# Performance work log

Hardware: AMD Instinct MI355X
Metric: run time of the kernel (lower is better)

## Reference

```python
import jax, jax.numpy as jnp
import numpy as np

N_NODES = 100000
N_GRAPHS = 256
EPS = 1e-5


def setup_inputs() -> dict:
    key = jax.random.key(0)
    ks = jax.random.split(key, 16)
    x = jax.random.normal(ks[0], (N_NODES, 7), dtype=jnp.float32)
    edge_index = jax.random.randint(ks[1], (2, 1600000), 0, N_NODES, dtype=jnp.int64)
    batch = jnp.sort(jax.random.randint(ks[2], (N_NODES,), 0, N_GRAPHS, dtype=jnp.int64))

    def lin(k, fi, fo):
        s = 1.0 / np.sqrt(fi)
        kw, kb = jax.random.split(k)
        W = jax.random.uniform(kw, (fi, fo), jnp.float32, -s, s)
        b = jax.random.uniform(kb, (fo,), jnp.float32, -s, s)
        return W, b

    W1, b1 = lin(ks[3], 7, 71)
    W2, b2 = lin(ks[4], 71, 135)
    W3, b3 = lin(ks[5], 135, 199)
    Wl1, bl1 = lin(ks[6], 199, 49)
    Wl2, bl2 = lin(ks[7], 49, 2)
    return {
        "x": x, "edge_index": edge_index, "batch": batch,
        "bn0_g": jnp.ones((7,)), "bn0_b": jnp.zeros((7,)),
        "bn1_g": jnp.ones((71,)), "bn1_b": jnp.zeros((71,)),
        "bn2_g": jnp.ones((135,)), "bn2_b": jnp.zeros((135,)),
        "W1": W1, "b1": b1, "W2": W2, "b2": b2, "W3": W3, "b3": b3,
        "Wl1": Wl1, "bl1": bl1, "Wl2": Wl2, "bl2": bl2,
    }


def _bn(x, g, b):
    # BatchNorm1d in training mode: batch stats over node dim
    m = jnp.mean(x, axis=0)
    v = jnp.mean(jnp.square(x - m), axis=0)
    return (x - m) * jax.lax.rsqrt(v + EPS) * g + b


def _gcn(x, src, dst, norm, W, b):
    # PyG GCNConv: x' = D^{-1/2} (A+I) D^{-1/2} (x W) + b
    h = x @ W
    out = jax.ops.segment_sum(norm[:, None] * h[src], dst, num_segments=N_NODES)
    return out + b


def reference(x, edge_index, batch, bn0_g, bn0_b, bn1_g, bn1_b, bn2_g, bn2_b,
              W1, b1, W2, b2, W3, b3, Wl1, bl1, Wl2, bl2):
    # add self loops
    loops = jnp.arange(N_NODES, dtype=edge_index.dtype)
    src = jnp.concatenate([edge_index[0], loops])
    dst = jnp.concatenate([edge_index[1], loops])
    deg = jax.ops.segment_sum(jnp.ones_like(dst, dtype=x.dtype), dst, num_segments=N_NODES)
    d_isqrt = jax.lax.rsqrt(jnp.maximum(deg, 1.0))
    norm = d_isqrt[src] * d_isqrt[dst]

    h = _bn(x, bn0_g, bn0_b)
    h = jax.nn.relu(_gcn(h, src, dst, norm, W1, b1))
    h = _bn(h, bn1_g, bn1_b)
    h = jax.nn.relu(_gcn(h, src, dst, norm, W2, b2))
    h = _bn(h, bn2_g, bn2_b)
    h = jax.nn.relu(_gcn(h, src, dst, norm, W3, b3))

    # global mean pool over graphs
    sums = jax.ops.segment_sum(h, batch, num_segments=N_GRAPHS)
    cnts = jax.ops.segment_sum(jnp.ones((h.shape[0],), h.dtype), batch, num_segments=N_GRAPHS)
    pooled = sums / jnp.maximum(cnts, 1.0)[:, None]

    out = pooled @ Wl1 + bl1
    out = out @ Wl2 + bl2
    return out
```

## Files before the change

kernel.cpp:

```cpp
#include <hip/hip_runtime.h>
#include <hip/hip_fp16.h>

#define EPSV 1e-5f
#define BIN_CH 4096
#define BCAP 8192

typedef _Float16 f16;
typedef f16 half8 __attribute__((ext_vector_type(8)));
typedef float f32x4 __attribute__((ext_vector_type(4)));


__global__ __launch_bounds__(256) void k_bin(const int* __restrict__ src,
                                             const int* __restrict__ dst, int E, int EN,
                                             int NBK, int* __restrict__ gcur,
                                             int* __restrict__ binned) {
    __shared__ int cnt[512];
    __shared__ int base[512];
    for (int b = threadIdx.x; b < 512; b += 256) cnt[b] = 0;
    __syncthreads();
    int i0 = blockIdx.x * BIN_CH;
    int i1 = i0 + BIN_CH; if (i1 > EN) i1 = EN;
    for (int i = i0 + threadIdx.x; i < i1; i += 256) {
        int d = (i < E) ? dst[i] : (i - E);
        atomicAdd(&cnt[d >> 8], 1);
    }
    __syncthreads();
    for (int b = threadIdx.x; b < NBK; b += 256)
        if (cnt[b]) base[b] = b * BCAP + atomicAdd(&gcur[b], cnt[b]);
    __syncthreads();
    for (int i = i0 + threadIdx.x; i < i1; i += 256) {
        int s, d;
        if (i < E) { s = src[i]; d = dst[i]; }
        else       { s = i - E; d = s; }
        int pos = atomicAdd(&base[d >> 8], 1);
        binned[pos] = s | ((d & 255) << 24);
    }
}

__global__ __launch_bounds__(256) void k_bucket(const int* __restrict__ binned,
                                                const int* __restrict__ gcur, int N,
                                                int* __restrict__ deg, int* __restrict__ rs,
                                                int* __restrict__ csr_s,
                                                float* __restrict__ disq) {
    __shared__ int deg_l[256];
    __shared__ int sc[256];
    __shared__ int cur_l[256];
    int b = blockIdx.x;
    int t = threadIdx.x;
    int start = b * BCAP, end = start + gcur[b];
    deg_l[t] = 0;
    __syncthreads();
    for (int i = start + t; i < end; i += 256)
        atomicAdd(&deg_l[((unsigned)binned[i]) >> 24], 1);
    __syncthreads();
    sc[t] = deg_l[t];
    __syncthreads();
    for (int off = 1; off < 256; off <<= 1) {
        int v = (t >= off) ? sc[t - off] : 0;
        __syncthreads();
        sc[t] += v;
        __syncthreads();
    }
    int rs_l = sc[t] - deg_l[t];
    int n = b * 256 + t;
    if (n < N) {
        deg[n] = deg_l[t];
        rs[n] = start + rs_l;
        disq[n] = rsqrtf((float)(deg_l[t] > 0 ? deg_l[t] : 1));
    }
    cur_l[t] = start + rs_l;
    __syncthreads();
    for (int i = start + t; i < end; i += 256) {
        int p = binned[i];
        int loc = ((unsigned)p) >> 24;
        int idx = atomicAdd(&cur_l[loc], 1);
        csr_s[idx] = p & 0xFFFFFF;
    }
}

__global__ __launch_bounds__(256) void k_wfill(const int* __restrict__ rs,
                                               const int* __restrict__ deg,
                                               const int* __restrict__ csr_s,
                                               const float* __restrict__ disq,
                                               int2* __restrict__ csr_sw, int N) {
    int wave = threadIdx.x >> 6, lane = threadIdx.x & 63;
    int n = blockIdx.x * 4 + wave;
    if (n >= N) return;
    int e0 = rs[n], dg = deg[n];
    float dn = disq[n];
    for (int j = lane; j < dg; j += 64) {
        int s = csr_s[e0 + j];
        int2 sw;
        sw.x = s;
        sw.y = __float_as_int(disq[s] * dn);
        csr_sw[e0 + j] = sw;
    }
}


__global__ __launch_bounds__(256) void k_prep(
    const float* __restrict__ colsum, const float* __restrict__ colsq,
    const float* __restrict__ g, const float* __restrict__ b, float invN,
    const float* __restrict__ W, int Cin, int Cout, int KP,
    f16* __restrict__ Wp, float* __restrict__ wrow) {
    __shared__ float lsc[192];
    __shared__ float lsh[192];
    __shared__ float red[4];
    int t = threadIdx.x;
    int c = blockIdx.x;
    if (t < KP) {
        float scv = 0.f, shv = 0.f;
        if (t < Cin) {
            float m = colsum[t] * invN;
            float v = colsq[t] * invN - m * m;
            float rstd = rsqrtf(fmaxf(v, 0.f) + EPSV);
            scv = rstd * g[t];
            shv = b[t] - m * scv;
        }
        lsc[t] = scv; lsh[t] = shv;
    }
    __syncthreads();
    float part = 0.f;
    if (t < KP) {
        float wv = (t < Cin && c < Cout) ? W[(size_t)t * Cout + c] : 0.f;
        Wp[(size_t)c * KP + t] = (f16)(lsc[t] * wv);
        part = lsh[t] * wv;
    }
    for (int off = 32; off > 0; off >>= 1) part += __shfl_down(part, off);
    int lane = t & 63, wid = t >> 6;
    if (lane == 0) red[wid] = part;
    __syncthreads();
    if (t == 0) wrow[c] = red[0] + red[1] + red[2] + red[3];
}


__global__ __launch_bounds__(256) void k_padx_stats(const float* __restrict__ x,
                                                    __half* __restrict__ xp, int N,
                                                    float* __restrict__ colsum,
                                                    float* __restrict__ colsq,
                                                    const int* __restrict__ batch,
                                                    int* __restrict__ gstart,
                                                    int* __restrict__ gend) {
    __shared__ float ls[16];
    int t = threadIdx.x;
    int n = blockIdx.x * 256 + t;
    int lane = t & 63;
    if (t < 16) ls[t] = 0.f;
    __syncthreads();
    float v[7] = {0.f, 0.f, 0.f, 0.f, 0.f, 0.f, 0.f};
    if (n < N) {
#pragma unroll
        for (int j = 0; j < 7; ++j) v[j] = x[(size_t)n * 7 + j];
        __half h[8];
#pragma unroll
        for (int j = 0; j < 7; ++j) h[j] = __float2half(v[j]);
        h[7] = __float2half(0.f);
        *(float4*)(xp + (size_t)n * 8) = *(float4*)h;
        int g = batch[n];
        int gp = (n == 0) ? -1 : batch[n - 1];
        if (gp != g) gstart[g] = n;
        int gn = (n == N - 1) ? -1 : batch[n + 1];
        if (gn != g) gend[g] = n + 1;
    }
#pragma unroll
    for (int j = 0; j < 7; ++j) {
        float s = v[j];
        float q = v[j] * v[j];
        for (int off = 32; off > 0; off >>= 1) {
            s += __shfl_down(s, off);
            q += __shfl_down(q, off);
        }
        if (lane == 0) {
            atomicAdd(&ls[j], s);
            atomicAdd(&ls[8 + j], q);
        }
    }
    __syncthreads();
    if (t < 8)               atomicAdd(&colsum[t], ls[t]);
    else if (t < 16)         atomicAdd(&colsq[t - 8], ls[t]);
}


__global__ void k_gather8(const __half* __restrict__ xp, const int2* __restrict__ csr_sw,
                          const int* __restrict__ rs, const int* __restrict__ deg,
                          __half* __restrict__ out, float* __restrict__ rsum, int N) {
    int n = blockIdx.x * blockDim.x + threadIdx.x;
    if (n >= N) return;
    int e0 = rs[n], eend = e0 + deg[n];
    float a0 = 0.f, a1 = 0.f, a2 = 0.f, a3 = 0.f, a4 = 0.f, a5 = 0.f, a6 = 0.f, a7 = 0.f;
    float ws = 0.f;
    for (int e = e0; e < eend; ++e) {
        int2 sw = csr_sw[e];
        float w = __int_as_float(sw.y);
        ws += w;
        float4 r = *(const float4*)(xp + (size_t)sw.x * 8);
        const __half2* hh = (const __half2*)&r;
        float2 q0 = __half22float2(hh[0]);
        float2 q1 = __half22float2(hh[1]);
        float2 q2 = __half22float2(hh[2]);
        float2 q3 = __half22float2(hh[3]);
        a0 = fmaf(w, q0.x, a0); a1 = fmaf(w, q0.y, a1);
        a2 = fmaf(w, q1.x, a2); a3 = fmaf(w, q1.y, a3);
        a4 = fmaf(w, q2.x, a4); a5 = fmaf(w, q2.y, a5);
        a6 = fmaf(w, q3.x, a6); a7 = fmaf(w, q3.y, a7);
    }
    rsum[n] = ws;
    __half h[8];
    h[0] = __float2half(a0); h[1] = __float2half(a1);
    h[2] = __float2half(a2); h[3] = __float2half(a3);
    h[4] = __float2half(a4); h[5] = __float2half(a5);
    h[6] = __float2half(a6); h[7] = __float2half(a7);
    *(float4*)(out + (size_t)n * 8) = *(float4*)h;
}


__global__ __launch_bounds__(256) void k_gemm_mfma(
    const f16* __restrict__ A, int SPa,
    const f16* __restrict__ Bt, int KP,
    const float* __restrict__ rsum, const float* __restrict__ wrow,
    const float* __restrict__ bias,
    f16* __restrict__ outM, int SPm, int MAIN, f16* __restrict__ outT, int TOTW,
    float* __restrict__ colsum, float* __restrict__ colsq, int do_stats,
    int N, int Cout) {
    __shared__ f16 As[128][40];
    __shared__ float s_sum[64];
    __shared__ float s_sq[64];
    const int r0 = blockIdx.x * 128;
    const int c0 = blockIdx.y * 64;
    const int t = threadIdx.x;
    const int wave = t >> 6, lane = t & 63;
    const int l15 = lane & 15, quad = lane >> 4;

    if (t < 64) { s_sum[t] = 0.f; s_sq[t] = 0.f; }

    f32x4 zero4 = {0.f, 0.f, 0.f, 0.f};
    f32x4 acc[2][4];
#pragma unroll
    for (int mi = 0; mi < 2; ++mi)
#pragma unroll
        for (int ni = 0; ni < 4; ++ni) acc[mi][ni] = zero4;

    const int KT = KP >> 5;
    for (int kt = 0; kt < KT; ++kt) {
        int k0 = kt * 32;
        {
            int kcol = (t & 7) * 4;
            int rbase = t >> 3;
            int gk = k0 + kcol;
            bool kok = (gk + 4 <= SPa);
#pragma unroll
            for (int i = 0; i < 4; ++i) {
                int row = rbase + i * 32;
                int gr = r0 + row;
                ushort4 v = {0, 0, 0, 0};
                if (gr < N && kok)
                    v = *(const ushort4*)(A + (size_t)gr * SPa + gk);
                *(ushort4*)&As[row][kcol] = v;
            }
        }
        __syncthreads();
        half8 a0 = *(const half8*)&As[wave * 32 + l15][quad * 8];
        half8 a1 = *(const half8*)&As[wave * 32 + 16 + l15][quad * 8];
#pragma unroll
        for (int ni = 0; ni < 4; ++ni) {
            half8 b = *(const half8*)(Bt + (size_t)(c0 + ni * 16 + l15) * KP + k0 + quad * 8);
            acc[0][ni] = __builtin_amdgcn_mfma_f32_16x16x32_f16(a0, b, acc[0][ni], 0, 0, 0);
            acc[1][ni] = __builtin_amdgcn_mfma_f32_16x16x32_f16(a1, b, acc[1][ni], 0, 0, 0);
        }
        __syncthreads();
    }

    float wr[4], bi[4];
#pragma unroll
    for (int ni = 0; ni < 4; ++ni) {
        int gc = c0 + ni * 16 + l15;
        wr[ni] = wrow[gc];
        bi[ni] = (gc < Cout) ? bias[gc] : 0.f;
    }
    float ps[4] = {}, pq[4] = {};
#pragma unroll
    for (int mi = 0; mi < 2; ++mi) {
#pragma unroll
        for (int reg = 0; reg < 4; ++reg) {
            int gr = r0 + wave * 32 + mi * 16 + quad * 4 + reg;
            if (gr >= N) continue;
            float rsv = rsum[gr];
#pragma unroll
            for (int ni = 0; ni < 4; ++ni) {
                int gc = c0 + ni * 16 + l15;
                float o = acc[mi][ni][reg] + rsv * wr[ni] + bi[ni];
                o = fmaxf(o, 0.f);
                if (gc >= Cout) o = 0.f;
                ps[ni] += o; pq[ni] += o * o;
                if (gc < MAIN) {
                    if (gc < TOTW) outM[(size_t)gr * SPm + gc] = (f16)o;
                } else if (gc < TOTW) {
                    outT[(size_t)gr * 8 + (gc - MAIN)] = (f16)o;
                }
            }
        }
    }
    if (do_stats) {
#pragma unroll
        for (int ni = 0; ni < 4; ++ni) {
            int cl = ni * 16 + l15;
            atomicAdd(&s_sum[cl], ps[ni]);
            atomicAdd(&s_sq[cl], pq[ni]);
        }
        __syncthreads();
        if (t < 64 && c0 + t < Cout) {
            atomicAdd(&colsum[c0 + t], s_sum[t]);
            atomicAdd(&colsq[c0 + t], s_sq[t]);
        }
    }
}

__device__ __forceinline__ void fma8(float* acc, float w, float4 r) {
    float2 q0 = __half22float2(((const __half2*)&r)[0]);
    float2 q1 = __half22float2(((const __half2*)&r)[1]);
    float2 q2 = __half22float2(((const __half2*)&r)[2]);
    float2 q3 = __half22float2(((const __half2*)&r)[3]);
    acc[0] = fmaf(w, q0.x, acc[0]); acc[1] = fmaf(w, q0.y, acc[1]);
    acc[2] = fmaf(w, q1.x, acc[2]); acc[3] = fmaf(w, q1.y, acc[3]);
    acc[4] = fmaf(w, q2.x, acc[4]); acc[5] = fmaf(w, q2.y, acc[5]);
    acc[6] = fmaf(w, q3.x, acc[6]); acc[7] = fmaf(w, q3.y, acc[7]);
}

__device__ __forceinline__ void gather_walk(const __half* __restrict__ gb, int SPM,
                                            const int2* __restrict__ csr_sw,
                                            int e0, int eend, float* acc) {
    if (e0 >= eend) return;
    int2 cur[8];
#pragma unroll
    for (int i = 0; i < 8; ++i) cur[i] = csr_sw[e0 + i];
    for (int e = e0; e < eend; ) {
        int en = e + 8;
        int2 nxt[8];
#pragma unroll
        for (int i = 0; i < 8; ++i) nxt[i] = csr_sw[en + i];
        float4 r[8];
#pragma unroll
        for (int i = 0; i < 8; ++i) {
            int si = (e + i < eend) ? cur[i].x : 0;
            r[i] = *(const float4*)(gb + (size_t)si * SPM);
        }
#pragma unroll
        for (int i = 0; i < 8; ++i) {
            float w = (e + i < eend) ? __int_as_float(cur[i].y) : 0.f;
            fma8(acc, w, r[i]);
        }
#pragma unroll
        for (int i = 0; i < 8; ++i) cur[i] = nxt[i];
        e = en;
    }
}


__global__ __launch_bounds__(256) void k_fused2(
    const __half* __restrict__ Am, const __half* __restrict__ At,
    const f16* __restrict__ Bt,
    const int* __restrict__ rs, const int* __restrict__ deg,
    const int2* __restrict__ csr_sw,
    const float* __restrict__ rsum, const float* __restrict__ wrow,
    const float* __restrict__ bias,
    f16* __restrict__ outM, f16* __restrict__ outT,
    float* __restrict__ colsum, float* __restrict__ colsq, int N) {
    const int KP = 96, ASW = 104, SPM = 64, COUT = 135;
    __shared__ f16 As[64][104];
    __shared__ float rsum_l[64];
    const int r0 = blockIdx.x * 64;
    const int t = threadIdx.x;
    const int wave = t >> 6, lane = t & 63;
    const int l15 = lane & 15, quad = lane >> 4;

    if (t < 64) rsum_l[t] = (r0 + t < N) ? rsum[r0 + t] : 0.f;
    {
        float4 z = {0.f, 0.f, 0.f, 0.f};
        for (int i = t; i < 64 * ASW / 8; i += 256) ((float4*)As)[i] = z;
    }
    __syncthreads();

    {
        const int sub = lane >> 3, lsub = lane & 7;
        const __half* gb = Am + lsub * 8;
        for (int pass = 0; pass < 2; ++pass) {
            int lrow = wave * 16 + pass * 8 + sub;
            int n = r0 + lrow;
            float acc[8] = {};
            if (n < N) gather_walk(gb, SPM, csr_sw, rs[n], rs[n] + deg[n], acc);
            __half2 h[4];
            h[0] = __floats2half2_rn(acc[0], acc[1]);
            h[1] = __floats2half2_rn(acc[2], acc[3]);
            h[2] = __floats2half2_rn(acc[4], acc[5]);
            h[3] = __floats2half2_rn(acc[6], acc[7]);
            *(float4*)&As[lrow][lsub * 8] = *(float4*)h;
        }
    }
    {
        const int p = lane >> 2, sl = lane & 3;
        int lrow = wave * 16 + p;
        int n = r0 + lrow;
        float acc[8] = {};
        if (n < N) {
            int eend = rs[n] + deg[n];
            for (int e = rs[n] + sl; e < eend; e += 4) {
                int2 sw = csr_sw[e];
                fma8(acc, __int_as_float(sw.y), *(const float4*)(At + (size_t)sw.x * 8));
            }
        }
#pragma unroll
        for (int j = 0; j < 8; ++j) {
            acc[j] += __shfl_xor(acc[j], 1);
            acc[j] += __shfl_xor(acc[j], 2);
        }
        if (sl == 0) {
            __half2 h[4];
            h[0] = __floats2half2_rn(acc[0], acc[1]);
            h[1] = __floats2half2_rn(acc[2], acc[3]);
            h[2] = __floats2half2_rn(acc[4], acc[5]);
            h[3] = __floats2half2_rn(acc[6], acc[7]);
            *(float4*)&As[lrow][64] = *(float4*)h;
        }
    }
    __syncthreads();

    for (int ch = 0; ch < 3; ++ch) {
        const int gc = wave * 48 + ch * 16 + l15;
        f32x4 zero4 = {0.f, 0.f, 0.f, 0.f};
        f32x4 acc2[4];
#pragma unroll
        for (int mg = 0; mg < 4; ++mg) acc2[mg] = zero4;
#pragma unroll
        for (int kt = 0; kt < 3; ++kt) {
            int k0 = kt * 32;
            half8 b = *(const half8*)(Bt + (size_t)gc * KP + k0 + quad * 8);
#pragma unroll
            for (int mg = 0; mg < 4; ++mg) {
                half8 a = *(const half8*)&As[mg * 16 + l15][k0 + quad * 8];
                acc2[mg] = __builtin_amdgcn_mfma_f32_16x16x32_f16(a, b, acc2[mg], 0, 0, 0);
            }
        }
        float wr1 = wrow[gc];
        float bi1 = (gc < COUT) ? bias[gc] : 0.f;
        float ps = 0.f, pq = 0.f;
#pragma unroll
        for (int mg = 0; mg < 4; ++mg) {
#pragma unroll
            for (int reg = 0; reg < 4; ++reg) {
                int lrow = mg * 16 + quad * 4 + reg;
                int gr = r0 + lrow;
                float o = acc2[mg][reg] + rsum_l[lrow] * wr1 + bi1;
                o = fmaxf(o, 0.f);
                if (gc >= COUT || gr >= N) o = 0.f;
                ps += o; pq += o * o;
                if (gr < N) {
                    if (gc < 128)      outM[(size_t)gr * 128 + gc] = (f16)o;
                    else if (gc < 136) outT[(size_t)gr * 8 + (gc - 128)] = (f16)o;
                }
            }
        }
        ps += __shfl_down(ps, 32); ps += __shfl_down(ps, 16);
        pq += __shfl_down(pq, 32); pq += __shfl_down(pq, 16);
        if (lane < 16 && gc < COUT) {
            atomicAdd(&colsum[gc], ps);
            atomicAdd(&colsq[gc], pq);
        }
    }
}


__global__ __launch_bounds__(256) void k_fused3(
    const __half* __restrict__ Am, const __half* __restrict__ At,
    const f16* __restrict__ Bt,
    const int* __restrict__ rs, const int* __restrict__ deg,
    const int2* __restrict__ csr_sw,
    const float* __restrict__ rsum, const float* __restrict__ wrow,
    const float* __restrict__ bias, const int* __restrict__ batch,
    float* __restrict__ pooled, int N) {
    const int KP = 160, ASW = 168, SPM = 128, COUT = 199;
    __shared__ f16 As[64][168];
    __shared__ int sbat[64];
    __shared__ float rsum_l[64];
    const int r0 = blockIdx.x * 64;
    const int t = threadIdx.x;
    const int wave = t >> 6, lane = t & 63;
    const int l15 = lane & 15, quad = lane >> 4;

    if (t < 64) {
        int gr = r0 + t;
        sbat[t] = batch[(gr < N) ? gr : (N - 1)];
        rsum_l[t] = (gr < N) ? rsum[gr] : 0.f;
    }
    {
        float4 z = {0.f, 0.f, 0.f, 0.f};
        for (int i = t; i < 64 * ASW / 8; i += 256) ((float4*)As)[i] = z;
    }
    __syncthreads();

    {
        const int sub = lane >> 4, lsub = lane & 15;
        const __half* gb = Am + lsub * 8;
        for (int pass = 0; pass < 4; ++pass) {
            int lrow = wave * 16 + pass * 4 + sub;
            int n = r0 + lrow;
            float acc[8] = {};
            if (n < N) gather_walk(gb, SPM, csr_sw, rs[n], rs[n] + deg[n], acc);
            __half2 h[4];
            h[0] = __floats2half2_rn(acc[0], acc[1]);
            h[1] = __floats2half2_rn(acc[2], acc[3]);
            h[2] = __floats2half2_rn(acc[4], acc[5]);
            h[3] = __floats2half2_rn(acc[6], acc[7]);
            *(float4*)&As[lrow][lsub * 8] = *(float4*)h;
        }
    }
    {
        const int p = lane >> 2, sl = lane & 3;
        int lrow = wave * 16 + p;
        int n = r0 + lrow;
        float acc[8] = {};
        if (n < N) {
            int eend = rs[n] + deg[n];
            for (int e = rs[n] + sl; e < eend; e += 4) {
                int2 sw = csr_sw[e];
                fma8(acc, __int_as_float(sw.y), *(const float4*)(At + (size_t)sw.x * 8));
            }
        }
#pragma unroll
        for (int j = 0; j < 8; ++j) {
            acc[j] += __shfl_xor(acc[j], 1);
            acc[j] += __shfl_xor(acc[j], 2);
        }
        if (sl == 0) {
            __half2 h[4];
            h[0] = __floats2half2_rn(acc[0], acc[1]);
            h[1] = __floats2half2_rn(acc[2], acc[3]);
            h[2] = __floats2half2_rn(acc[4], acc[5]);
            h[3] = __floats2half2_rn(acc[6], acc[7]);
            *(float4*)&As[lrow][128] = *(float4*)h;
        }
    }
    __syncthreads();

    const int g0 = sbat[0];
    const int ng = sbat[63] - g0;
    unsigned gpack = 0;
#pragma unroll
    for (int i = 0; i < 16; ++i) {
        int lrow = (i >> 2) * 16 + quad * 4 + (i & 3);
        gpack |= (unsigned)(sbat[lrow] - g0) << (2 * i);
    }

    for (int ch = 0; ch < 2; ++ch) {
        const int cb = wave * 64 + ch * 32;
        f32x4 zero4 = {0.f, 0.f, 0.f, 0.f};
        f32x4 acc2[4][2];
#pragma unroll
        for (int mg = 0; mg < 4; ++mg) {
            acc2[mg][0] = zero4; acc2[mg][1] = zero4;
        }
#pragma unroll
        for (int kt = 0; kt < 5; ++kt) {
            int k0 = kt * 32;
            half8 b0 = *(const half8*)(Bt + (size_t)(cb + l15) * KP + k0 + quad * 8);
            half8 b1 = *(const half8*)(Bt + (size_t)(cb + 16 + l15) * KP + k0 + quad * 8);
#pragma unroll
            for (int mg = 0; mg < 4; ++mg) {
                half8 a = *(const half8*)&As[mg * 16 + l15][k0 + quad * 8];
                acc2[mg][0] = __builtin_amdgcn_mfma_f32_16x16x32_f16(a, b0, acc2[mg][0], 0, 0, 0);
                acc2[mg][1] = __builtin_amdgcn_mfma_f32_16x16x32_f16(a, b1, acc2[mg][1], 0, 0, 0);
            }
        }
        float wr[2], bi[2];
        int gcn[2];
#pragma unroll
        for (int ni = 0; ni < 2; ++ni) {
            gcn[ni] = cb + ni * 16 + l15;
            wr[ni] = wrow[gcn[ni]];
            bi[ni] = (gcn[ni] < COUT) ? bias[gcn[ni]] : 0.f;
        }
#pragma unroll
        for (int mg = 0; mg < 4; ++mg) {
#pragma unroll
            for (int reg = 0; reg < 4; ++reg) {
                int lrow = mg * 16 + quad * 4 + reg;
                bool rok = (r0 + lrow < N);
                float rsv = rsum_l[lrow];
#pragma unroll
                for (int ni = 0; ni < 2; ++ni) {
                    float o = acc2[mg][ni][reg] + rsv * wr[ni] + bi[ni];
                    o = fmaxf(o, 0.f);
                    acc2[mg][ni][reg] = (rok && gcn[ni] < COUT) ? o : 0.f;
                }
            }
        }
        for (int gg = 0; gg <= ng; ++gg) {
            float p0 = 0.f, p1 = 0.f;
#pragma unroll
            for (int i = 0; i < 16; ++i) {
                bool m = (((gpack >> (2 * i)) & 3u) == (unsigned)gg);
                int mg = i >> 2, reg = i & 3;
                p0 += m ? acc2[mg][0][reg] : 0.f;
                p1 += m ? acc2[mg][1][reg] : 0.f;
            }
            p0 += __shfl_down(p0, 32); p0 += __shfl_down(p0, 16);
            p1 += __shfl_down(p1, 32); p1 += __shfl_down(p1, 16);
            if (lane < 16) {
                int g = g0 + gg;
                if (gcn[0] < COUT && p0 != 0.f)
                    atomicAdd(&pooled[(size_t)g * COUT + gcn[0]], p0);
                if (gcn[1] < COUT && p1 != 0.f)
                    atomicAdd(&pooled[(size_t)g * COUT + gcn[1]], p1);
            }
        }
    }
}


__global__ void k_mlp(const float* __restrict__ pooled, const int* __restrict__ gstart,
                      const int* __restrict__ gend,
                      const float* __restrict__ Wl1, const float* __restrict__ bl1,
                      const float* __restrict__ Wl2, const float* __restrict__ bl2,
                      float* __restrict__ out, int C) {
    __shared__ float p[199];
    __shared__ float t1[49];
    int g = blockIdx.x;
    int cnt = gend[g] - gstart[g];
    float inv = 1.f / (float)(cnt > 1 ? cnt : 1);
    for (int k = threadIdx.x; k < C; k += blockDim.x) p[k] = pooled[g * C + k] * inv;
    __syncthreads();
    if (threadIdx.x < 49) {
        float acc = bl1[threadIdx.x];
        for (int k = 0; k < C; ++k) acc += p[k] * Wl1[k * 49 + threadIdx.x];
        t1[threadIdx.x] = acc;
    }
    __syncthreads();
    if (threadIdx.x < 2) {
        float acc = bl2[threadIdx.x];
        for (int k = 0; k < 49; ++k) acc += t1[k] * Wl2[k * 2 + threadIdx.x];
        out[g * 2 + threadIdx.x] = acc;
    }
}


extern "C" void kernel_launch(void* const* d_in, const int* in_sizes, int n_in,
                              void* d_out, int out_size, void* d_ws, size_t ws_size,
                              hipStream_t stream) {
    const float* x     = (const float*)d_in[0];
    const int*   ei    = (const int*)d_in[1];
    const int*   batch = (const int*)d_in[2];
    const float* bn0g = (const float*)d_in[3];
    const float* bn0b = (const float*)d_in[4];
    const float* bn1g = (const float*)d_in[5];
    const float* bn1b = (const float*)d_in[6];
    const float* bn2g = (const float*)d_in[7];
    const float* bn2b = (const float*)d_in[8];
    const float* W1  = (const float*)d_in[9];
    const float* b1  = (const float*)d_in[10];
    const float* W2  = (const float*)d_in[11];
    const float* b2  = (const float*)d_in[12];
    const float* W3  = (const float*)d_in[13];
    const float* b3  = (const float*)d_in[14];
    const float* Wl1 = (const float*)d_in[15];
    const float* bl1 = (const float*)d_in[16];
    const float* Wl2 = (const float*)d_in[17];
    const float* bl2 = (const float*)d_in[18];

    const int N = in_sizes[0] / 7;
    const int E = in_sizes[1] / 2;
    const int EN = E + N;
    const int G = out_size / 2;
    const int NB = (N + 255) / 256;
    const int NBK = (N + 255) / 256;
    const int NBIN = (EN + BIN_CH - 1) / BIN_CH;

    const int* src = ei;
    const int* dst = ei + E;

    char* w = (char*)d_ws;
    auto alloc = [&](size_t bytes) -> void* {
        void* p = (void*)w;
        w += ((bytes + 255) / 256) * 256;
        return p;
    };
    size_t szH1m = (size_t)N * 64 * sizeof(__half);
    size_t szH1t = (size_t)N * 8 * sizeof(__half);
    size_t szH2m = (size_t)N * 128 * sizeof(__half);
    size_t szH2t = (size_t)N * 8 * sizeof(__half);
    char* regA = (char*)alloc(szH1m + szH1t + szH2m + szH2t);
    __half* H1m = (__half*)regA;
    __half* H1t = (__half*)(regA + szH1m);
    __half* H2m = (__half*)(regA + szH1m + szH1t);
    __half* H2t = (__half*)(regA + szH1m + szH1t + szH2m);

    __half* bufG = (__half*)alloc((size_t)N * 8 * sizeof(__half));
    f16*    wp   = (f16*)  alloc((size_t)256 * 160 * sizeof(f16));
    float*  wrow = (float*)alloc(256 * sizeof(float));
    __half* xp   = (__half*)alloc((size_t)N * 8 * sizeof(__half));
    float* disq  = (float*)alloc((size_t)N * sizeof(float));
    float* rsum  = (float*)alloc((size_t)N * sizeof(float));
    int*   deg   = (int*)  alloc((size_t)N * sizeof(int));
    int*   rs    = (int*)  alloc((size_t)N * sizeof(int));
    int*   binned= (int*)  alloc((size_t)NBK * BCAP * sizeof(int));
    int*   csr_s = (int*)  alloc((size_t)NBK * BCAP * sizeof(int));
    int2*  csr_sw= (int2*) alloc((size_t)NBK * BCAP * sizeof(int2) + 256);
    float* colsum0 = (float*)alloc(256 * sizeof(float));
    float* colsq0  = (float*)alloc(256 * sizeof(float));
    float* colsumA = (float*)alloc(256 * sizeof(float));
    float* colsqA  = (float*)alloc(256 * sizeof(float));
    float* colsumB = (float*)alloc(256 * sizeof(float));
    float* colsqB  = (float*)alloc(256 * sizeof(float));
    int*   gcur    = (int*)  alloc(512 * sizeof(int));
    float* pooled  = (float*)alloc((size_t)G * 199 * sizeof(float));
    int*   gstart  = (int*)  alloc((size_t)G * sizeof(int));
    int*   gend    = (int*)  alloc((size_t)G * sizeof(int));

    size_t zbytes = 6 * 1024 + 2048 + (((size_t)G * 199 * sizeof(float) + 255) / 256) * 256;
    hipMemsetAsync(colsum0, 0, zbytes, stream);

    k_bin<<<NBIN, 256, 0, stream>>>(src, dst, E, EN, NBK, gcur, binned);
    k_bucket<<<NBK, 256, 0, stream>>>(binned, gcur, N, deg, rs, csr_s, disq);
    k_wfill<<<(N + 3) / 4, 256, 0, stream>>>(rs, deg, csr_s, disq, csr_sw, N);

    const int GB = (N + 127) / 128;
    const int GB64 = (N + 63) / 64;

    k_padx_stats<<<NB, 256, 0, stream>>>(x, xp, N, colsum0, colsq0, batch, gstart, gend);
    k_prep<<<128, 256, 0, stream>>>(colsum0, colsq0, bn0g, bn0b, 1.f / (float)N,
                                    W1, 7, 71, 32, wp, wrow);
    k_gather8<<<(N + 255) / 256, 256, 0, stream>>>(xp, csr_sw, rs, deg, bufG, rsum, N);
    {
        dim3 grid(GB, 2);
        k_gemm_mfma<<<grid, 256, 0, stream>>>((const f16*)bufG, 8, wp, 32, rsum, wrow, b1,
                                              (f16*)H1m, 64, 64, (f16*)H1t, 72,
                                              colsumA, colsqA, 1, N, 71);
    }
    k_prep<<<192, 256, 0, stream>>>(colsumA, colsqA, bn1g, bn1b, 1.f / (float)N,
                                    W2, 71, 135, 96, wp, wrow);
    k_fused2<<<GB64, 256, 0, stream>>>(H1m, H1t, wp, rs, deg, csr_sw,
                                       rsum, wrow, b2, (f16*)H2m, (f16*)H2t,
                                       colsumB, colsqB, N);
    k_prep<<<256, 256, 0, stream>>>(colsumB, colsqB, bn2g, bn2b, 1.f / (float)N,
                                    W3, 135, 199, 160, wp, wrow);
    k_fused3<<<GB64, 256, 0, stream>>>(H2m, H2t, wp, rs, deg, csr_sw,
                                       rsum, wrow, b3, batch, pooled, N);

    k_mlp<<<G, 64, 0, stream>>>(pooled, gstart, gend, Wl1, bl1, Wl2, bl2, (float*)d_out, 199);
}
```

Before: 442.9 us.

## Fuse layer-1 gather with MFMA GEMM and shrink fused tiles to 32 rows

Replaces the separate layer-1 gather kernel and MFMA GEMM kernel with one fused kernel. It gathers the 8-wide inputs into shared memory using 8 lanes per node, then runs the 71-column MFMA epilogue directly, so the intermediate buffer is never written to or read back from global memory. The fused2/fused3 kernels move from 64-row to 32-row tiles with launch_bounds(256,8), 8-lane tail gathers and a 6-deep edge prefetch instead of 8. This aims for more blocks and higher occupancy, at the cost of re-reading the weights in more blocks and issuing more atomics.

```diff
diff --git a/kernel.cpp b/kernel.cpp
--- a/kernel.cpp
+++ b/kernel.cpp
@@ -180,141 +180,6 @@
     else if (t < 16)         atomicAdd(&colsq[t - 8], ls[t]);
 }
 
-
-__global__ void k_gather8(const __half* __restrict__ xp, const int2* __restrict__ csr_sw,
-                          const int* __restrict__ rs, const int* __restrict__ deg,
-                          __half* __restrict__ out, float* __restrict__ rsum, int N) {
-    int n = blockIdx.x * blockDim.x + threadIdx.x;
-    if (n >= N) return;
-    int e0 = rs[n], eend = e0 + deg[n];
-    float a0 = 0.f, a1 = 0.f, a2 = 0.f, a3 = 0.f, a4 = 0.f, a5 = 0.f, a6 = 0.f, a7 = 0.f;
-    float ws = 0.f;
-    for (int e = e0; e < eend; ++e) {
-        int2 sw = csr_sw[e];
-        float w = __int_as_float(sw.y);
-        ws += w;
-        float4 r = *(const float4*)(xp + (size_t)sw.x * 8);
-        const __half2* hh = (const __half2*)&r;
-        float2 q0 = __half22float2(hh[0]);
-        float2 q1 = __half22float2(hh[1]);
-        float2 q2 = __half22float2(hh[2]);
-        float2 q3 = __half22float2(hh[3]);
-        a0 = fmaf(w, q0.x, a0); a1 = fmaf(w, q0.y, a1);
-        a2 = fmaf(w, q1.x, a2); a3 = fmaf(w, q1.y, a3);
-        a4 = fmaf(w, q2.x, a4); a5 = fmaf(w, q2.y, a5);
-        a6 = fmaf(w, q3.x, a6); a7 = fmaf(w, q3.y, a7);
-    }
-    rsum[n] = ws;
-    __half h[8];
-    h[0] = __float2half(a0); h[1] = __float2half(a1);
-    h[2] = __float2half(a2); h[3] = __float2half(a3);
-    h[4] = __float2half(a4); h[5] = __float2half(a5);
-    h[6] = __float2half(a6); h[7] = __float2half(a7);
-    *(float4*)(out + (size_t)n * 8) = *(float4*)h;
-}
-
-
-__global__ __launch_bounds__(256) void k_gemm_mfma(
-    const f16* __restrict__ A, int SPa,
-    const f16* __restrict__ Bt, int KP,
-    const float* __restrict__ rsum, const float* __restrict__ wrow,
-    const float* __restrict__ bias,
-    f16* __restrict__ outM, int SPm, int MAIN, f16* __restrict__ outT, int TOTW,
-    float* __restrict__ colsum, float* __restrict__ colsq, int do_stats,
-    int N, int Cout) {
-    __shared__ f16 As[128][40];
-    __shared__ float s_sum[64];
-    __shared__ float s_sq[64];
-    const int r0 = blockIdx.x * 128;
-    const int c0 = blockIdx.y * 64;
-    const int t = threadIdx.x;
-    const int wave = t >> 6, lane = t & 63;
-    const int l15 = lane & 15, quad = lane >> 4;
-
-    if (t < 64) { s_sum[t] = 0.f; s_sq[t] = 0.f; }
-
-    f32x4 zero4 = {0.f, 0.f, 0.f, 0.f};
-    f32x4 acc[2][4];
-#pragma unroll
-    for (int mi = 0; mi < 2; ++mi)
-#pragma unroll
-        for (int ni = 0; ni < 4; ++ni) acc[mi][ni] = zero4;
-
-    const int KT = KP >> 5;
-    for (int kt = 0; kt < KT; ++kt) {
-        int k0 = kt * 32;
-        {
-            int kcol = (t & 7) * 4;
-            int rbase = t >> 3;
-            int gk = k0 + kcol;
-            bool kok = (gk + 4 <= SPa);
-#pragma unroll
-            for (int i = 0; i < 4; ++i) {
-                int row = rbase + i * 32;
-                int gr = r0 + row;
-                ushort4 v = {0, 0, 0, 0};
-                if (gr < N && kok)
-                    v = *(const ushort4*)(A + (size_t)gr * SPa + gk);
-                *(ushort4*)&As[row][kcol] = v;
-            }
-        }
-        __syncthreads();
-        half8 a0 = *(const half8*)&As[wave * 32 + l15][quad * 8];
-        half8 a1 = *(const half8*)&As[wave * 32 + 16 + l15][quad * 8];
-#pragma unroll
-        for (int ni = 0; ni < 4; ++ni) {
-            half8 b = *(const half8*)(Bt + (size_t)(c0 + ni * 16 + l15) * KP + k0 + quad * 8);
-            acc[0][ni] = __builtin_amdgcn_mfma_f32_16x16x32_f16(a0, b, acc[0][ni], 0, 0, 0);
-            acc[1][ni] = __builtin_amdgcn_mfma_f32_16x16x32_f16(a1, b, acc[1][ni], 0, 0, 0);
-        }
-        __syncthreads();
-    }
-
-    float wr[4], bi[4];
-#pragma unroll
-    for (int ni = 0; ni < 4; ++ni) {
-        int gc = c0 + ni * 16 + l15;
-        wr[ni] = wrow[gc];
-        bi[ni] = (gc < Cout) ? bias[gc] : 0.f;
-    }
-    float ps[4] = {}, pq[4] = {};
-#pragma unroll
-    for (int mi = 0; mi < 2; ++mi) {
-#pragma unroll
-        for (int reg = 0; reg < 4; ++reg) {
-            int gr = r0 + wave * 32 + mi * 16 + quad * 4 + reg;
-            if (gr >= N) continue;
-            float rsv = rsum[gr];
-#pragma unroll
-            for (int ni = 0; ni < 4; ++ni) {
-                int gc = c0 + ni * 16 + l15;
-                float o = acc[mi][ni][reg] + rsv * wr[ni] + bi[ni];
-                o = fmaxf(o, 0.f);
-                if (gc >= Cout) o = 0.f;
-                ps[ni] += o; pq[ni] += o * o;
-                if (gc < MAIN) {
-                    if (gc < TOTW) outM[(size_t)gr * SPm + gc] = (f16)o;
-                } else if (gc < TOTW) {
-                    outT[(size_t)gr * 8 + (gc - MAIN)] = (f16)o;
-                }
-            }
-        }
-    }
-    if (do_stats) {
-#pragma unroll
-        for (int ni = 0; ni < 4; ++ni) {
-            int cl = ni * 16 + l15;
-            atomicAdd(&s_sum[cl], ps[ni]);
-            atomicAdd(&s_sq[cl], pq[ni]);
-        }
-        __syncthreads();
-        if (t < 64 && c0 + t < Cout) {
-            atomicAdd(&colsum[c0 + t], s_sum[t]);
-            atomicAdd(&colsq[c0 + t], s_sq[t]);
-        }
-    }
-}
-
 __device__ __forceinline__ void fma8(float* acc, float w, float4 r) {
     float2 q0 = __half22float2(((const __half2*)&r)[0]);
     float2 q1 = __half22float2(((const __half2*)&r)[1]);
@@ -330,33 +195,129 @@
                                             const int2* __restrict__ csr_sw,
                                             int e0, int eend, float* acc) {
     if (e0 >= eend) return;
-    int2 cur[8];
-#pragma unroll
-    for (int i = 0; i < 8; ++i) cur[i] = csr_sw[e0 + i];
+    int2 cur[6];
+#pragma unroll
+    for (int i = 0; i < 6; ++i) cur[i] = csr_sw[e0 + i];
     for (int e = e0; e < eend; ) {
-        int en = e + 8;
-        int2 nxt[8];
-#pragma unroll
-        for (int i = 0; i < 8; ++i) nxt[i] = csr_sw[en + i];
-        float4 r[8];
-#pragma unroll
-        for (int i = 0; i < 8; ++i) {
+        int en = e + 6;
+        int2 nxt[6];
+#pragma unroll
+        for (int i = 0; i < 6; ++i) nxt[i] = csr_sw[en + i];
+        float4 r[6];
+#pragma unroll
+        for (int i = 0; i < 6; ++i) {
             int si = (e + i < eend) ? cur[i].x : 0;
             r[i] = *(const float4*)(gb + (size_t)si * SPM);
         }
 #pragma unroll
-        for (int i = 0; i < 8; ++i) {
+        for (int i = 0; i < 6; ++i) {
             float w = (e + i < eend) ? __int_as_float(cur[i].y) : 0.f;
             fma8(acc, w, r[i]);
         }
 #pragma unroll
-        for (int i = 0; i < 8; ++i) cur[i] = nxt[i];
+        for (int i = 0; i < 6; ++i) cur[i] = nxt[i];
         e = en;
     }
 }
 
 
-__global__ __launch_bounds__(256) void k_fused2(
+__global__ __launch_bounds__(256, 8) void k_fused1(
+    const __half* __restrict__ xp, const f16* __restrict__ Bt,
+    const int* __restrict__ rs, const int* __restrict__ deg,
+    const int2* __restrict__ csr_sw,
+    const float* __restrict__ wrow, const float* __restrict__ bias,
+    f16* __restrict__ outM, f16* __restrict__ outT,
+    float* __restrict__ colsum, float* __restrict__ colsq,
+    float* __restrict__ rsum, int N) {
+    const int COUT = 71;
+    __shared__ f16 As[32][40];
+    __shared__ float rsum_l[32];
+    const int r0 = blockIdx.x * 32;
+    const int t = threadIdx.x;
+    const int wave = t >> 6, lane = t & 63;
+    const int l15 = lane & 15, quad = lane >> 4;
+
+    {
+        float4 z = {0.f, 0.f, 0.f, 0.f};
+        for (int i = t; i < 32 * 40 / 8; i += 256) ((float4*)As)[i] = z;
+    }
+    __syncthreads();
+
+    {
+        int lrow = wave * 8 + (lane >> 3);
+        int sl = lane & 7;
+        int n = r0 + lrow;
+        float acc[8] = {};
+        float ws = 0.f;
+        if (n < N) {
+            int eend = rs[n] + deg[n];
+            for (int e = rs[n] + sl; e < eend; e += 8) {
+                int2 sw = csr_sw[e];
+                float w = __int_as_float(sw.y);
+                ws += w;
+                fma8(acc, w, *(const float4*)(xp + (size_t)sw.x * 8));
+            }
+        }
+#pragma unroll
+        for (int j = 0; j < 8; ++j) {
+            acc[j] += __shfl_xor(acc[j], 1);
+            acc[j] += __shfl_xor(acc[j], 2);
+            acc[j] += __shfl_xor(acc[j], 4);
+        }
+        ws += __shfl_xor(ws, 1); ws += __shfl_xor(ws, 2); ws += __shfl_xor(ws, 4);
+        if (sl == 0) {
+            __half2 h[4];
+            h[0] = __floats2half2_rn(acc[0], acc[1]);
+            h[1] = __floats2half2_rn(acc[2], acc[3]);
+            h[2] = __floats2half2_rn(acc[4], acc[5]);
+            h[3] = __floats2half2_rn(acc[6], acc[7]);
+            *(float4*)&As[lrow][0] = *(float4*)h;
+            rsum_l[lrow] = ws;
+            if (n < N) rsum[n] = ws;
+        }
+    }
+    __syncthreads();
+
+    for (int c16 = wave; c16 < 5; c16 += 4) {
+        const int gc = c16 * 16 + l15;
+        f32x4 zero4 = {0.f, 0.f, 0.f, 0.f};
+        f32x4 acc2[2] = {zero4, zero4};
+        half8 b = *(const half8*)(Bt + (size_t)gc * 32 + quad * 8);
+#pragma unroll
+        for (int mg = 0; mg < 2; ++mg) {
+            half8 a = *(const half8*)&As[mg * 16 + l15][quad * 8];
+            acc2[mg] = __builtin_amdgcn_mfma_f32_16x16x32_f16(a, b, acc2[mg], 0, 0, 0);
+        }
+        float wr1 = wrow[gc];
+        float bi1 = (gc < COUT) ? bias[gc] : 0.f;
+        float ps = 0.f, pq = 0.f;
+#pragma unroll
+        for (int mg = 0; mg < 2; ++mg) {
+#pragma unroll
+            for (int reg = 0; reg < 4; ++reg) {
+                int lrow = mg * 16 + quad * 4 + reg;
+                int gr = r0 + lrow;
+                float o = acc2[mg][reg] + rsum_l[lrow] * wr1 + bi1;
+                o = fmaxf(o, 0.f);
+                if (gc >= COUT || gr >= N) o = 0.f;
+                ps += o; pq += o * o;
+                if (gr < N) {
+                    if (gc < 64)      outM[(size_t)gr * 64 + gc] = (f16)o;
+                    else if (gc < 72) outT[(size_t)gr * 8 + (gc - 64)] = (f16)o;
+                }
+            }
+        }
+        ps += __shfl_down(ps, 32); ps += __shfl_down(ps, 16);
+        pq += __shfl_down(pq, 32); pq += __shfl_down(pq, 16);
+        if (lane < 16 && gc < COUT) {
+            atomicAdd(&colsum[gc], ps);
+            atomicAdd(&colsq[gc], pq);
+        }
+    }
+}
+
+
+__global__ __launch_bounds__(256, 8) void k_fused2(
     const __half* __restrict__ Am, const __half* __restrict__ At,
     const f16* __restrict__ Bt,
     const int* __restrict__ rs, const int* __restrict__ deg,
@@ -365,45 +326,42 @@
     const float* __restrict__ bias,
     f16* __restrict__ outM, f16* __restrict__ outT,
     float* __restrict__ colsum, float* __restrict__ colsq, int N) {
-    const int KP = 96, ASW = 104, SPM = 64, COUT = 135;
-    __shared__ f16 As[64][104];
-    __shared__ float rsum_l[64];
-    const int r0 = blockIdx.x * 64;
+    const int KP = 96, SPM = 64, COUT = 135;
+    __shared__ f16 As[32][104];
+    __shared__ float rsum_l[32];
+    const int r0 = blockIdx.x * 32;
     const int t = threadIdx.x;
     const int wave = t >> 6, lane = t & 63;
     const int l15 = lane & 15, quad = lane >> 4;
 
-    if (t < 64) rsum_l[t] = (r0 + t < N) ? rsum[r0 + t] : 0.f;
+    if (t < 32) rsum_l[t] = (r0 + t < N) ? rsum[r0 + t] : 0.f;
     {
         float4 z = {0.f, 0.f, 0.f, 0.f};
-        for (int i = t; i < 64 * ASW / 8; i += 256) ((float4*)As)[i] = z;
-    }
-    __syncthreads();
-
-    {
-        const int sub = lane >> 3, lsub = lane & 7;
-        const __half* gb = Am + lsub * 8;
-        for (int pass = 0; pass < 2; ++pass) {
-            int lrow = wave * 16 + pass * 8 + sub;
-            int n = r0 + lrow;
-            float acc[8] = {};
-            if (n < N) gather_walk(gb, SPM, csr_sw, rs[n], rs[n] + deg[n], acc);
-            __half2 h[4];
-            h[0] = __floats2half2_rn(acc[0], acc[1]);
-            h[1] = __floats2half2_rn(acc[2], acc[3]);
-            h[2] = __floats2half2_rn(acc[4], acc[5]);
-            h[3] = __floats2half2_rn(acc[6], acc[7]);
-            *(float4*)&As[lrow][lsub * 8] = *(float4*)h;
-        }
-    }
-    {
-        const int p = lane >> 2, sl = lane & 3;
-        int lrow = wave * 16 + p;
+        for (int i = t; i < 32 * 104 / 8; i += 256) ((float4*)As)[i] = z;
+    }
+    __syncthreads();
+
+    {
+        int lrow = wave * 8 + (lane >> 3);
+        const __half* gb = Am + (lane & 7) * 8;
+        int n = r0 + lrow;
+        float acc[8] = {};
+        if (n < N) gather_walk(gb, SPM, csr_sw, rs[n], rs[n] + deg[n], acc);
+        __half2 h[4];
+        h[0] = __floats2half2_rn(acc[0], acc[1]);
+        h[1] = __floats2half2_rn(acc[2], acc[3]);
+        h[2] = __floats2half2_rn(acc[4], acc[5]);
+        h[3] = __floats2half2_rn(acc[6], acc[7]);
+        *(float4*)&As[lrow][(lane & 7) * 8] = *(float4*)h;
+    }
+    {
+        int lrow = wave * 8 + (lane >> 3);
+        int sl = lane & 7;
         int n = r0 + lrow;
         float acc[8] = {};
         if (n < N) {
             int eend = rs[n] + deg[n];
-            for (int e = rs[n] + sl; e < eend; e += 4) {
+            for (int e = rs[n] + sl; e < eend; e += 8) {
                 int2 sw = csr_sw[e];
                 fma8(acc, __int_as_float(sw.y), *(const float4*)(At + (size_t)sw.x * 8));
             }
@@ -412,6 +370,7 @@
         for (int j = 0; j < 8; ++j) {
             acc[j] += __shfl_xor(acc[j], 1);
             acc[j] += __shfl_xor(acc[j], 2);
+            acc[j] += __shfl_xor(acc[j], 4);
         }
         if (sl == 0) {
             __half2 h[4];
@@ -424,18 +383,16 @@
     }
     __syncthreads();
 
-    for (int ch = 0; ch < 3; ++ch) {
-        const int gc = wave * 48 + ch * 16 + l15;
+    for (int c16 = wave; c16 < 9; c16 += 4) {
+        const int gc = c16 * 16 + l15;
         f32x4 zero4 = {0.f, 0.f, 0.f, 0.f};
-        f32x4 acc2[4];
-#pragma unroll
-        for (int mg = 0; mg < 4; ++mg) acc2[mg] = zero4;
+        f32x4 acc2[2] = {zero4, zero4};
 #pragma unroll
         for (int kt = 0; kt < 3; ++kt) {
             int k0 = kt * 32;
             half8 b = *(const half8*)(Bt + (size_t)gc * KP + k0 + quad * 8);
 #pragma unroll
-            for (int mg = 0; mg < 4; ++mg) {
+            for (int mg = 0; mg < 2; ++mg) {
                 half8 a = *(const half8*)&As[mg * 16 + l15][k0 + quad * 8];
                 acc2[mg] = __builtin_amdgcn_mfma_f32_16x16x32_f16(a, b, acc2[mg], 0, 0, 0);
             }
@@ -444,7 +401,7 @@
         float bi1 = (gc < COUT) ? bias[gc] : 0.f;
         float ps = 0.f, pq = 0.f;
 #pragma unroll
-        for (int mg = 0; mg < 4; ++mg) {
+        for (int mg = 0; mg < 2; ++mg) {
 #pragma unroll
             for (int reg = 0; reg < 4; ++reg) {
                 int lrow = mg * 16 + quad * 4 + reg;
@@ -469,7 +426,7 @@
 }
 
 
-__global__ __launch_bounds__(256) void k_fused3(
+__global__ __launch_bounds__(256, 8) void k_fused3(
     const __half* __restrict__ Am, const __half* __restrict__ At,
     const f16* __restrict__ Bt,
     const int* __restrict__ rs, const int* __restrict__ deg,
@@ -477,31 +434,31 @@
     const float* __restrict__ rsum, const float* __restrict__ wrow,
     const float* __restrict__ bias, const int* __restrict__ batch,
     float* __restrict__ pooled, int N) {
-    const int KP = 160, ASW = 168, SPM = 128, COUT = 199;
-    __shared__ f16 As[64][168];
-    __shared__ int sbat[64];
-    __shared__ float rsum_l[64];
-    const int r0 = blockIdx.x * 64;
+    const int KP = 160, SPM = 128, COUT = 199;
+    __shared__ f16 As[32][168];
+    __shared__ int sbat[32];
+    __shared__ float rsum_l[32];
+    const int r0 = blockIdx.x * 32;
     const int t = threadIdx.x;
     const int wave = t >> 6, lane = t & 63;
     const int l15 = lane & 15, quad = lane >> 4;
 
-    if (t < 64) {
+    if (t < 32) {
         int gr = r0 + t;
         sbat[t] = batch[(gr < N) ? gr : (N - 1)];
         rsum_l[t] = (gr < N) ? rsum[gr] : 0.f;
     }
     {
         float4 z = {0.f, 0.f, 0.f, 0.f};
-        for (int i = t; i < 64 * ASW / 8; i += 256) ((float4*)As)[i] = z;
+        for (int i = t; i < 32 * 168 / 8; i += 256) ((float4*)As)[i] = z;
     }
     __syncthreads();
 
     {
         const int sub = lane >> 4, lsub = lane & 15;
         const __half* gb = Am + lsub * 8;
-        for (int pass = 0; pass < 4; ++pass) {
-            int lrow = wave * 16 + pass * 4 + sub;
+        for (int pass = 0; pass < 2; ++pass) {
+            int lrow = wave * 8 + pass * 4 + sub;
             int n = r0 + lrow;
             float acc[8] = {};
             if (n < N) gather_walk(gb, SPM, csr_sw, rs[n], rs[n] + deg[n], acc);
@@ -514,13 +471,13 @@
         }
     }
     {
-        const int p = lane >> 2, sl = lane & 3;
-        int lrow = wave * 16 + p;
+        int lrow = wave * 8 + (lane >> 3);
+        int sl = lane & 7;
         int n = r0 + lrow;
         float acc[8] = {};
         if (n < N) {
             int eend = rs[n] + deg[n];
-            for (int e = rs[n] + sl; e < eend; e += 4) {
+            for (int e = rs[n] + sl; e < eend; e += 8) {
                 int2 sw = csr_sw[e];
                 fma8(acc, __int_as_float(sw.y), *(const float4*)(At + (size_t)sw.x * 8));
             }
@@ -529,6 +486,7 @@
         for (int j = 0; j < 8; ++j) {
             acc[j] += __shfl_xor(acc[j], 1);
             acc[j] += __shfl_xor(acc[j], 2);
+            acc[j] += __shfl_xor(acc[j], 4);
         }
         if (sl == 0) {
             __half2 h[4];
@@ -542,75 +500,51 @@
     __syncthreads();
 
     const int g0 = sbat[0];
-    const int ng = sbat[63] - g0;
+    const int ng = sbat[31] - g0;
     unsigned gpack = 0;
 #pragma unroll
-    for (int i = 0; i < 16; ++i) {
+    for (int i = 0; i < 8; ++i) {
         int lrow = (i >> 2) * 16 + quad * 4 + (i & 3);
         gpack |= (unsigned)(sbat[lrow] - g0) << (2 * i);
     }
 
-    for (int ch = 0; ch < 2; ++ch) {
-        const int cb = wave * 64 + ch * 32;
+    for (int c16 = wave; c16 < 13; c16 += 4) {
+        const int gc = c16 * 16 + l15;
         f32x4 zero4 = {0.f, 0.f, 0.f, 0.f};
-        f32x4 acc2[4][2];
-#pragma unroll
-        for (int mg = 0; mg < 4; ++mg) {
-            acc2[mg][0] = zero4; acc2[mg][1] = zero4;
-        }
+        f32x4 acc2[2] = {zero4, zero4};
 #pragma unroll
         for (int kt = 0; kt < 5; ++kt) {
             int k0 = kt * 32;
-            half8 b0 = *(const half8*)(Bt + (size_t)(cb + l15) * KP + k0 + quad * 8);
-            half8 b1 = *(const half8*)(Bt + (size_t)(cb + 16 + l15) * KP + k0 + quad * 8);
-#pragma unroll
-            for (int mg = 0; mg < 4; ++mg) {
+            half8 b = *(const half8*)(Bt + (size_t)gc * KP + k0 + quad * 8);
+#pragma unroll
+            for (int mg = 0; mg < 2; ++mg) {
                 half8 a = *(const half8*)&As[mg * 16 + l15][k0 + quad * 8];
-                acc2[mg][0] = __builtin_amdgcn_mfma_f32_16x16x32_f16(a, b0, acc2[mg][0], 0, 0, 0);
-                acc2[mg][1] = __builtin_amdgcn_mfma_f32_16x16x32_f16(a, b1, acc2[mg][1], 0, 0, 0);
-            }
-        }
-        float wr[2], bi[2];
-        int gcn[2];
-#pragma unroll
-        for (int ni = 0; ni < 2; ++ni) {
-            gcn[ni] = cb + ni * 16 + l15;
-            wr[ni] = wrow[gcn[ni]];
-            bi[ni] = (gcn[ni] < COUT) ? bias[gcn[ni]] : 0.f;
-        }
-#pragma unroll
-        for (int mg = 0; mg < 4; ++mg) {
+                acc2[mg] = __builtin_amdgcn_mfma_f32_16x16x32_f16(a, b, acc2[mg], 0, 0, 0);
+            }
+        }
+        float wr1 = wrow[gc];
+        float bi1 = (gc < COUT) ? bias[gc] : 0.f;
+#pragma unroll
+        for (int mg = 0; mg < 2; ++mg) {
 #pragma unroll
             for (int reg = 0; reg < 4; ++reg) {
                 int lrow = mg * 16 + quad * 4 + reg;
                 bool rok = (r0 + lrow < N);
-                float rsv = rsum_l[lrow];
-#pragma unroll
-                for (int ni = 0; ni < 2; ++ni) {
-                    float o = acc2[mg][ni][reg] + rsv * wr[ni] + bi[ni];
-                    o = fmaxf(o, 0.f);
-                    acc2[mg][ni][reg] = (rok && gcn[ni] < COUT) ? o : 0.f;
-                }
+                float o = acc2[mg][reg] + rsum_l[lrow] * wr1 + bi1;
+                o = fmaxf(o, 0.f);
+                acc2[mg][reg] = (rok && gc < COUT) ? o : 0.f;
             }
         }
         for (int gg = 0; gg <= ng; ++gg) {
-            float p0 = 0.f, p1 = 0.f;
-#pragma unroll
-            for (int i = 0; i < 16; ++i) {
+            float p = 0.f;
+#pragma unroll
+            for (int i = 0; i < 8; ++i) {
                 bool m = (((gpack >> (2 * i)) & 3u) == (unsigned)gg);
-                int mg = i >> 2, reg = i & 3;
-                p0 += m ? acc2[mg][0][reg] : 0.f;
-                p1 += m ? acc2[mg][1][reg] : 0.f;
-            }
-            p0 += __shfl_down(p0, 32); p0 += __shfl_down(p0, 16);
-            p1 += __shfl_down(p1, 32); p1 += __shfl_down(p1, 16);
-            if (lane < 16) {
-                int g = g0 + gg;
-                if (gcn[0] < COUT && p0 != 0.f)
-                    atomicAdd(&pooled[(size_t)g * COUT + gcn[0]], p0);
-                if (gcn[1] < COUT && p1 != 0.f)
-                    atomicAdd(&pooled[(size_t)g * COUT + gcn[1]], p1);
-            }
+                p += m ? acc2[i >> 2][i & 3] : 0.f;
+            }
+            p += __shfl_down(p, 32); p += __shfl_down(p, 16);
+            if (lane < 16 && gc < COUT && p != 0.f)
+                atomicAdd(&pooled[(size_t)(g0 + gg) * COUT + gc], p);
         }
     }
 }
@@ -692,7 +626,6 @@
     __half* H2m = (__half*)(regA + szH1m + szH1t);
     __half* H2t = (__half*)(regA + szH1m + szH1t + szH2m);
 
-    __half* bufG = (__half*)alloc((size_t)N * 8 * sizeof(__half));
     f16*    wp   = (f16*)  alloc((size_t)256 * 160 * sizeof(f16));
     float*  wrow = (float*)alloc(256 * sizeof(float));
     __half* xp   = (__half*)alloc((size_t)N * 8 * sizeof(__half));
@@ -721,27 +654,21 @@
     k_bucket<<<NBK, 256, 0, stream>>>(binned, gcur, N, deg, rs, csr_s, disq);
     k_wfill<<<(N + 3) / 4, 256, 0, stream>>>(rs, deg, csr_s, disq, csr_sw, N);
 
-    const int GB = (N + 127) / 128;
-    const int GB64 = (N + 63) / 64;
+    const int GB32 = (N + 31) / 32;
 
     k_padx_stats<<<NB, 256, 0, stream>>>(x, xp, N, colsum0, colsq0, batch, gstart, gend);
     k_prep<<<128, 256, 0, stream>>>(colsum0, colsq0, bn0g, bn0b, 1.f / (float)N,
                                     W1, 7, 71, 32, wp, wrow);
-    k_gather8<<<(N + 255) / 256, 256, 0, stream>>>(xp, csr_sw, rs, deg, bufG, rsum, N);
-    {
-        dim3 grid(GB, 2);
-        k_gemm_mfma<<<grid, 256, 0, stream>>>((const f16*)bufG, 8, wp, 32, rsum, wrow, b1,
-                                              (f16*)H1m, 64, 64, (f16*)H1t, 72,
-                                              colsumA, colsqA, 1, N, 71);
-    }
+    k_fused1<<<GB32, 256, 0, stream>>>(xp, wp, rs, deg, csr_sw, wrow, b1,
+                                       (f16*)H1m, (f16*)H1t, colsumA, colsqA, rsum, N);
     k_prep<<<192, 256, 0, stream>>>(colsumA, colsqA, bn1g, bn1b, 1.f / (float)N,
                                     W2, 71, 135, 96, wp, wrow);
-    k_fused2<<<GB64, 256, 0, stream>>>(H1m, H1t, wp, rs, deg, csr_sw,
+    k_fused2<<<GB32, 256, 0, stream>>>(H1m, H1t, wp, rs, deg, csr_sw,
                                        rsum, wrow, b2, (f16*)H2m, (f16*)H2t,
                                        colsumB, colsqB, N);
     k_prep<<<256, 256, 0, stream>>>(colsumB, colsqB, bn2g, bn2b, 1.f / (float)N,
                                     W3, 135, 199, 160, wp, wrow);
-    k_fused3<<<GB64, 256, 0, stream>>>(H2m, H2t, wp, rs, deg, csr_sw,
+    k_fused3<<<GB32, 256, 0, stream>>>(H2m, H2t, wp, rs, deg, csr_sw,
                                        rsum, wrow, b3, batch, pooled, N);
 
     k_mlp<<<G, 64, 0, stream>>>(pooled, gstart, gend, Wl1, bl1, Wl2, bl2, (float*)d_out, 199);
```

New measurement: 526.4 us. 1.19x slower.
